# Kernel tuning notes

Hardware: AMD Instinct MI355X
Metric: run time of the kernel (lower is better)

## Reference

```python
import jax, jax.numpy as jnp
import numpy as np

N_NODES = 100000
N_EDGES = 600000
H_DIM = 128


def _gcn_layer(h, src, dst, norm, W, b):
    # m = (h @ W) * norm  -> scatter-sum over edges -> * norm + b -> LeakyReLU(0.2)
    m = jnp.matmul(h, W) * norm                      # [N, H]
    agg = jax.ops.segment_sum(m[src], dst, num_segments=N_NODES)  # [N, H]
    n = agg * norm + b
    return jnp.where(n > 0, n, 0.2 * n)


def setup_inputs() -> dict:
    key = jax.random.key(0)
    ks = jax.random.split(key, 8)
    node_id = jax.random.randint(ks[0], (N_NODES,), 0, N_NODES)
    src = jax.random.randint(ks[1], (N_EDGES,), 0, N_NODES)
    dst = jax.random.randint(ks[2], (N_EDGES,), 0, N_NODES)
    norm = jax.random.uniform(ks[3], (N_NODES, 1), dtype=jnp.float32)
    embed = jax.random.normal(ks[4], (N_NODES, H_DIM), dtype=jnp.float32) * 0.02
    embed = embed.at[0].set(0.0)  # padding_idx=0
    gain = np.sqrt(2.0)  # calculate_gain('relu')
    lim = gain * np.sqrt(6.0 / (H_DIM + H_DIM))
    W1 = jax.random.uniform(ks[5], (H_DIM, H_DIM), jnp.float32, -lim, lim)
    W2 = jax.random.uniform(ks[6], (H_DIM, H_DIM), jnp.float32, -lim, lim)
    stdv = 1.0 / np.sqrt(H_DIM)
    kb1, kb2 = jax.random.split(ks[7])
    b1 = jax.random.uniform(kb1, (H_DIM,), jnp.float32, -stdv, stdv)
    b2 = jax.random.uniform(kb2, (H_DIM,), jnp.float32, -stdv, stdv)
    return {"node_id": node_id, "src": src, "dst": dst, "norm": norm,
            "embed": embed, "W1": W1, "b1": b1, "W2": W2, "b2": b2}


def reference(node_id, src, dst, norm, embed, W1, b1, W2, b2):
    h = embed[node_id]                               # EmbeddingLayer
    h = _gcn_layer(h, src, dst, norm, W1, b1)        # GCNLayer 1
    h = _gcn_layer(h, src, dst, norm, W2, b2)        # GCNLayer 2
    return h
```

## Files before the change

kernel.cpp:

```cpp
#include <hip/hip_runtime.h>

namespace {
constexpr int NN = 100000;
constexpr int NE = 600000;
constexpr int H  = 128;
constexpr int SCAN_B = 256;
constexpr int NBLK_SCAN = (NN + SCAN_B - 1) / SCAN_B;

__global__ __launch_bounds__(256) void write_marker(float* __restrict__ out,
                                                    int n, float val) {
  int i = blockIdx.x * 256 + threadIdx.x;
  if (i < n) out[i] = val;
}


__global__ __launch_bounds__(256) void zero_f4(float4* __restrict__ p, int n4) {
  int i = blockIdx.x * 256 + threadIdx.x;
  if (i < n4) p[i] = float4{0.f, 0.f, 0.f, 0.f};
}

__global__ __launch_bounds__(256) void scatter_l1(
    const int* __restrict__ src, const int* __restrict__ dst,
    const int* __restrict__ node_id, const float* __restrict__ embed,
    const float* __restrict__ norm, float* __restrict__ agg) {
  int idx = blockIdx.x * 256 + threadIdx.x;
  int e = idx >> 5;
  if (e >= NE) return;
  int c = (idx & 31) << 2;
  int s = src[e];
  float nrm = norm[s];
  const float4 v = *reinterpret_cast<const float4*>(embed + (size_t)node_id[s] * H + c);
  float* o = agg + (size_t)dst[e] * H + c;
  atomicAdd(o + 0, v.x * nrm);
  atomicAdd(o + 1, v.y * nrm);
  atomicAdd(o + 2, v.z * nrm);
  atomicAdd(o + 3, v.w * nrm);
}

__global__ __launch_bounds__(256) void scatter_l2(
    const int* __restrict__ src, const int* __restrict__ dst,
    const float* __restrict__ h1, const float* __restrict__ norm,
    float* __restrict__ agg) {
  int idx = blockIdx.x * 256 + threadIdx.x;
  int e = idx >> 5;
  if (e >= NE) return;
  int c = (idx & 31) << 2;
  int s = src[e];
  float nrm = norm[s];
  const float4 v = *reinterpret_cast<const float4*>(h1 + (size_t)s * H + c);
  float* o = agg + (size_t)dst[e] * H + c;
  atomicAdd(o + 0, v.x * nrm);
  atomicAdd(o + 1, v.y * nrm);
  atomicAdd(o + 2, v.z * nrm);
  atomicAdd(o + 3, v.w * nrm);
}

__global__ __launch_bounds__(128) void row_gemm_act(
    const float* __restrict__ agg, const float* __restrict__ W,
    const float* __restrict__ norm, const float* __restrict__ bias,
    float* __restrict__ out) {
  __shared__ float hs[H];
  const int row = blockIdx.x, j = threadIdx.x;
  hs[j] = agg[(size_t)row * H + j];
  __syncthreads();
  float acc = 0.f;
#pragma unroll
  for (int k = 0; k < H; ++k) acc += hs[k] * W[k * H + j];
  float v = acc * norm[row] + bias[j];
  v = v > 0.f ? v : 0.2f * v;
  out[(size_t)row * H + j] = v;
}


__global__ __launch_bounds__(256) void zero_int(int* __restrict__ p, int n) {
  int i = blockIdx.x * 256 + threadIdx.x;
  if (i < n) p[i] = 0;
}

__global__ __launch_bounds__(256) void hist_dst(const int* __restrict__ dst,
                                                int* __restrict__ deg) {
  int e = blockIdx.x * 256 + threadIdx.x;
  if (e < NE) atomicAdd(&deg[dst[e]], 1);
}

__global__ __launch_bounds__(SCAN_B) void scan1(const int* __restrict__ deg,
                                                int* __restrict__ offs,
                                                int* __restrict__ bsums) {
  __shared__ int sh[SCAN_B];
  const int t = threadIdx.x;
  const int gid = blockIdx.x * SCAN_B + t;
  int v = (gid < NN) ? deg[gid] : 0;
  sh[t] = v;
  __syncthreads();
  for (int d = 1; d < SCAN_B; d <<= 1) {
    int add = (t >= d) ? sh[t - d] : 0;
    __syncthreads();
    sh[t] += add;
    __syncthreads();
  }
  if (gid < NN) offs[gid] = sh[t] - v;
  if (t == SCAN_B - 1) bsums[blockIdx.x] = sh[t];
}

__global__ __launch_bounds__(512) void scan2(int* __restrict__ bsums) {
  __shared__ int sh[512];
  const int t = threadIdx.x;
  int v = (t < NBLK_SCAN) ? bsums[t] : 0;
  sh[t] = v;
  __syncthreads();
  for (int d = 1; d < 512; d <<= 1) {
    int add = (t >= d) ? sh[t - d] : 0;
    __syncthreads();
    sh[t] += add;
    __syncthreads();
  }
  if (t < NBLK_SCAN) bsums[t] = sh[t] - v;
}

__global__ __launch_bounds__(256) void scan3(int* __restrict__ offs,
                                             const int* __restrict__ bsums,
                                             int* __restrict__ cnt) {
  int gid = blockIdx.x * 256 + threadIdx.x;
  if (gid < NN) {
    int v = offs[gid] + bsums[blockIdx.x];
    offs[gid] = v;
    cnt[gid] = v;
  }
  if (gid == 0) offs[NN] = NE;
}

template <bool WITH_REC>
__global__ __launch_bounds__(256) void fill_csr(
    const int* __restrict__ src, const int* __restrict__ dst,
    const int* __restrict__ node_id, const float* __restrict__ norm,
    int* __restrict__ cnt, int* __restrict__ csr2, int2* __restrict__ rec1) {
  int e = blockIdx.x * 256 + threadIdx.x;
  if (e >= NE) return;
  int d = dst[e];
  int s = src[e];
  int pos = atomicAdd(&cnt[d], 1);
  csr2[pos] = s;
  if (WITH_REC) rec1[pos] = make_int2(node_id[s], __float_as_int(norm[s]));
}


__global__ __launch_bounds__(256) void gather_rec(
    const int* __restrict__ offs, const int2* __restrict__ rec,
    const float* __restrict__ h, float* __restrict__ agg) {
  const int node = blockIdx.x * 8 + (threadIdx.x >> 5);
  const int c = (threadIdx.x & 31) << 2;
  const int beg = offs[node];
  const int end = offs[node + 1];
  float4 a0{0,0,0,0}, a1{0,0,0,0}, a2{0,0,0,0}, a3{0,0,0,0};
  int i = beg;
  for (; i + 4 <= end; i += 4) {
    int2 r0 = rec[i], r1 = rec[i + 1], r2 = rec[i + 2], r3 = rec[i + 3];
    const float4 v0 = *reinterpret_cast<const float4*>(h + (size_t)r0.x * H + c);
    const float4 v1 = *reinterpret_cast<const float4*>(h + (size_t)r1.x * H + c);
    const float4 v2 = *reinterpret_cast<const float4*>(h + (size_t)r2.x * H + c);
    const float4 v3 = *reinterpret_cast<const float4*>(h + (size_t)r3.x * H + c);
    float n0 = __int_as_float(r0.y), n1 = __int_as_float(r1.y);
    float n2 = __int_as_float(r2.y), n3 = __int_as_float(r3.y);
    a0.x += v0.x * n0; a0.y += v0.y * n0; a0.z += v0.z * n0; a0.w += v0.w * n0;
    a1.x += v1.x * n1; a1.y += v1.y * n1; a1.z += v1.z * n1; a1.w += v1.w * n1;
    a2.x += v2.x * n2; a2.y += v2.y * n2; a2.z += v2.z * n2; a2.w += v2.w * n2;
    a3.x += v3.x * n3; a3.y += v3.y * n3; a3.z += v3.z * n3; a3.w += v3.w * n3;
  }
  for (; i < end; ++i) {
    int2 r0 = rec[i];
    const float4 v0 = *reinterpret_cast<const float4*>(h + (size_t)r0.x * H + c);
    float n0 = __int_as_float(r0.y);
    a0.x += v0.x * n0; a0.y += v0.y * n0; a0.z += v0.z * n0; a0.w += v0.w * n0;
  }
  a0.x += a1.x + a2.x + a3.x;
  a0.y += a1.y + a2.y + a3.y;
  a0.z += a1.z + a2.z + a3.z;
  a0.w += a1.w + a2.w + a3.w;
  *reinterpret_cast<float4*>(agg + (size_t)node * H + c) = a0;
}

__global__ __launch_bounds__(256) void gather_idx(
    const int* __restrict__ offs, const int* __restrict__ csr,
    const float* __restrict__ h, float* __restrict__ agg) {
  const int node = blockIdx.x * 8 + (threadIdx.x >> 5);
  const int c = (threadIdx.x & 31) << 2;
  const int beg = offs[node];
  const int end = offs[node + 1];
  float4 a0{0,0,0,0}, a1{0,0,0,0}, a2{0,0,0,0}, a3{0,0,0,0};
  int i = beg;
  for (; i + 4 <= end; i += 4) {
    int s0 = csr[i], s1 = csr[i + 1], s2 = csr[i + 2], s3 = csr[i + 3];
    const float4 v0 = *reinterpret_cast<const float4*>(h + (size_t)s0 * H + c);
    const float4 v1 = *reinterpret_cast<const float4*>(h + (size_t)s1 * H + c);
    const float4 v2 = *reinterpret_cast<const float4*>(h + (size_t)s2 * H + c);
    const float4 v3 = *reinterpret_cast<const float4*>(h + (size_t)s3 * H + c);
    a0.x += v0.x; a0.y += v0.y; a0.z += v0.z; a0.w += v0.w;
    a1.x += v1.x; a1.y += v1.y; a1.z += v1.z; a1.w += v1.w;
    a2.x += v2.x; a2.y += v2.y; a2.z += v2.z; a2.w += v2.w;
    a3.x += v3.x; a3.y += v3.y; a3.z += v3.z; a3.w += v3.w;
  }
  for (; i < end; ++i) {
    int s0 = csr[i];
    const float4 v0 = *reinterpret_cast<const float4*>(h + (size_t)s0 * H + c);
    a0.x += v0.x; a0.y += v0.y; a0.z += v0.z; a0.w += v0.w;
  }
  a0.x += a1.x + a2.x + a3.x;
  a0.y += a1.y + a2.y + a3.y;
  a0.z += a1.z + a2.z + a3.z;
  a0.w += a1.w + a2.w + a3.w;
  *reinterpret_cast<float4*>(agg + (size_t)node * H + c) = a0;
}

__global__ __launch_bounds__(256) void gather_mid_l1(
    const int* __restrict__ offs, const int* __restrict__ csr,
    const int* __restrict__ node_id, const float* __restrict__ h,
    const float* __restrict__ norm, float* __restrict__ agg) {
  const int node = blockIdx.x * 8 + (threadIdx.x >> 5);
  const int c = (threadIdx.x & 31) << 2;
  const int beg = offs[node];
  const int end = offs[node + 1];
  float4 acc{0.f, 0.f, 0.f, 0.f};
  for (int i = beg; i < end; ++i) {
    int s = csr[i];
    float nrm = norm[s];
    const float4 v = *reinterpret_cast<const float4*>(h + (size_t)node_id[s] * H + c);
    acc.x += v.x * nrm; acc.y += v.y * nrm; acc.z += v.z * nrm; acc.w += v.w * nrm;
  }
  *reinterpret_cast<float4*>(agg + (size_t)node * H + c) = acc;
}


#define FMA4(ACC, S, W) \
  ACC.x += (S) * (W).x; ACC.y += (S) * (W).y; ACC.z += (S) * (W).z; ACC.w += (S) * (W).w;

template <bool SCALE_OUT>
__global__ __launch_bounds__(256, 2) void gemm_v5(
    const float* __restrict__ agg, const float* __restrict__ W,
    const float* __restrict__ norm, const float* __restrict__ bias,
    float* __restrict__ out) {
  const int t = threadIdx.x;
  const int rowBase = blockIdx.x * 128;
  const int j8 = t & 15;
  const int r0 = t >> 4;
  const float4* A4 = reinterpret_cast<const float4*>(agg) + (size_t)rowBase * 32;
  const float4* Wg = reinterpret_cast<const float4*>(W);

  float4 accA[8], accB[8];
#pragma unroll
  for (int i = 0; i < 8; ++i) {
    accA[i] = float4{0.f, 0.f, 0.f, 0.f};
    accB[i] = float4{0.f, 0.f, 0.f, 0.f};
  }

#pragma unroll 2
  for (int k4 = 0; k4 < 32; ++k4) {
    float4 a[8];
#pragma unroll
    for (int i = 0; i < 8; ++i) a[i] = A4[(r0 + 16 * i) * 32 + k4];
    const float4* wrow = Wg + k4 * 128 + 2 * j8;
    float4 wa0 = wrow[0],  wb0 = wrow[1];
    float4 wa1 = wrow[32], wb1 = wrow[33];
    float4 wa2 = wrow[64], wb2 = wrow[65];
    float4 wa3 = wrow[96], wb3 = wrow[97];
#pragma unroll
    for (int i = 0; i < 8; ++i) {
      FMA4(accA[i], a[i].x, wa0) FMA4(accB[i], a[i].x, wb0)
      FMA4(accA[i], a[i].y, wa1) FMA4(accB[i], a[i].y, wb1)
      FMA4(accA[i], a[i].z, wa2) FMA4(accB[i], a[i].z, wb2)
      FMA4(accA[i], a[i].w, wa3) FMA4(accB[i], a[i].w, wb3)
    }
  }

  const float4 bv0 = reinterpret_cast<const float4*>(bias)[2 * j8];
  const float4 bv1 = reinterpret_cast<const float4*>(bias)[2 * j8 + 1];
#pragma unroll
  for (int i = 0; i < 8; ++i) {
    const int row = rowBase + r0 + 16 * i;
    if (row < NN) {
      const float nrm = norm[row];
      float4 o0, o1;
      o0.x = accA[i].x * nrm + bv0.x; o0.y = accA[i].y * nrm + bv0.y;
      o0.z = accA[i].z * nrm + bv0.z; o0.w = accA[i].w * nrm + bv0.w;
      o1.x = accB[i].x * nrm + bv1.x; o1.y = accB[i].y * nrm + bv1.y;
      o1.z = accB[i].z * nrm + bv1.z; o1.w = accB[i].w * nrm + bv1.w;
      o0.x = o0.x > 0.f ? o0.x : 0.2f * o0.x;
      o0.y = o0.y > 0.f ? o0.y : 0.2f * o0.y;
      o0.z = o0.z > 0.f ? o0.z : 0.2f * o0.z;
      o0.w = o0.w > 0.f ? o0.w : 0.2f * o0.w;
      o1.x = o1.x > 0.f ? o1.x : 0.2f * o1.x;
      o1.y = o1.y > 0.f ? o1.y : 0.2f * o1.y;
      o1.z = o1.z > 0.f ? o1.z : 0.2f * o1.z;
      o1.w = o1.w > 0.f ? o1.w : 0.2f * o1.w;
      if (SCALE_OUT) {
        o0.x *= nrm; o0.y *= nrm; o0.z *= nrm; o0.w *= nrm;
        o1.x *= nrm; o1.y *= nrm; o1.z *= nrm; o1.w *= nrm;
      }
      float4* op = reinterpret_cast<float4*>(out + (size_t)row * H + j8 * 8);
      op[0] = o0;
      op[1] = o1;
    }
  }
}

}

extern "C" void kernel_launch(void* const* d_in, const int* in_sizes, int n_in,
                              void* d_out, int out_size, void* d_ws, size_t ws_size,
                              hipStream_t stream) {
  float* out = (float*)d_out;
  const int nElem = NN * H;
  const int mkBl  = (out_size + 255) / 256;

  bool order_ok =
      (n_in == 9 && in_sizes[0] == NN && in_sizes[1] == NE && in_sizes[2] == NE &&
       in_sizes[3] == NN && in_sizes[4] == NN * H && in_sizes[5] == H * H &&
       in_sizes[6] == H && in_sizes[7] == H * H && in_sizes[8] == H);
  if (!order_ok || out_size != nElem) {
    write_marker<<<mkBl, 256, 0, stream>>>(out, out_size,
                                           (out_size != nElem) ? 300.0f : 200.0f);
    return;
  }
  if (ws_size < (size_t)nElem * 4) {
    write_marker<<<mkBl, 256, 0, stream>>>(out, out_size,
                                           2.0f + (float)(ws_size >> 20));
    return;
  }

  const int* node_id = (const int*)d_in[0];
  const int* src     = (const int*)d_in[1];
  const int* dst     = (const int*)d_in[2];
  const float* norm  = (const float*)d_in[3];
  const float* embed = (const float*)d_in[4];
  const float* W1    = (const float*)d_in[5];
  const float* b1    = (const float*)d_in[6];
  const float* W2    = (const float*)d_in[7];
  const float* b2    = (const float*)d_in[8];

  float* agg = (float*)d_ws;
  float* h1n = out;
  int2* rec1 = (int2*)((char*)d_ws + (size_t)nElem * 4);
  int* csr2  = (int*)(rec1 + NE);
  int* offs  = csr2 + NE;
  int* cnt   = offs + (NN + 1);
  int* bsums = cnt + NN;

  const size_t need_mid =
      (size_t)nElem * 4 + ((size_t)NE + (NN + 1) + NN + 512) * 4;
  const size_t need_full = need_mid + (size_t)NE * 8;

  const int zeroNBl = (NN + 255) / 256;
  const int edgeBl  = (NE + 255) / 256;
  const int gemmBl  = (NN + 127) / 128;

  if (ws_size >= need_mid) {
    const bool full = (ws_size >= need_full);
    if (!full) {
      csr2  = (int*)((char*)d_ws + (size_t)nElem * 4);
      offs  = csr2 + NE;
      cnt   = offs + (NN + 1);
      bsums = cnt + NN;
    }

    zero_int<<<zeroNBl, 256, 0, stream>>>(cnt, NN);
    hist_dst<<<edgeBl, 256, 0, stream>>>(dst, cnt);
    scan1<<<NBLK_SCAN, SCAN_B, 0, stream>>>(cnt, offs, bsums);
    scan2<<<1, 512, 0, stream>>>(bsums);
    scan3<<<NBLK_SCAN, 256, 0, stream>>>(offs, bsums, cnt);
    if (full)
      fill_csr<true><<<edgeBl, 256, 0, stream>>>(src, dst, node_id, norm, cnt, csr2, rec1);
    else
      fill_csr<false><<<edgeBl, 256, 0, stream>>>(src, dst, node_id, norm, cnt, csr2, nullptr);

    if (full)
      gather_rec<<<NN / 8, 256, 0, stream>>>(offs, rec1, embed, agg);
    else
      gather_mid_l1<<<NN / 8, 256, 0, stream>>>(offs, csr2, node_id, embed, norm, agg);
    gemm_v5<true><<<gemmBl, 256, 0, stream>>>(agg, W1, norm, b1, h1n);

    gather_idx<<<NN / 8, 256, 0, stream>>>(offs, csr2, h1n, agg);
    gemm_v5<false><<<gemmBl, 256, 0, stream>>>(agg, W2, norm, b2, out);
    return;
  }

  const int zeroBl = (nElem / 4 + 255) / 256;
  const int scatBl = (NE * 32 + 255) / 256;

  zero_f4<<<zeroBl, 256, 0, stream>>>((float4*)agg, nElem / 4);
  scatter_l1<<<scatBl, 256, 0, stream>>>(src, dst, node_id, embed, norm, agg);
  row_gemm_act<<<NN, 128, 0, stream>>>(agg, W1, norm, b1, out);

  zero_f4<<<zeroBl, 256, 0, stream>>>((float4*)agg, nElem / 4);
  scatter_l2<<<scatBl, 256, 0, stream>>>(src, dst, out, norm, agg);
  row_gemm_act<<<NN, 128, 0, stream>>>(agg, W2, norm, b2, out);
}
```

Measured before the change: 421.7 us.

## Split GEMM output columns across two blocks and stage W half in LDS

Measured after the change: 371.0 us. 1.14x faster.

```diff
diff --git a/kernel.cpp b/kernel.cpp
--- a/kernel.cpp
+++ b/kernel.cpp
@@ -6,6 +6,7 @@
 constexpr int H  = 128;
 constexpr int SCAN_B = 256;
 constexpr int NBLK_SCAN = (NN + SCAN_B - 1) / SCAN_B;
+constexpr int NROWBLK = (NN + 127) / 128;
 
 __global__ __launch_bounds__(256) void write_marker(float* __restrict__ out,
                                                     int n, float val) {
@@ -234,36 +235,47 @@
   ACC.x += (S) * (W).x; ACC.y += (S) * (W).y; ACC.z += (S) * (W).z; ACC.w += (S) * (W).w;
 
 template <bool SCALE_OUT>
-__global__ __launch_bounds__(256, 2) void gemm_v5(
+__global__ __launch_bounds__(256, 3) void gemm_v6(
     const float* __restrict__ agg, const float* __restrict__ W,
     const float* __restrict__ norm, const float* __restrict__ bias,
     float* __restrict__ out) {
+  __shared__ float4 Wld[128 * 16];
   const int t = threadIdx.x;
-  const int rowBase = blockIdx.x * 128;
-  const int j8 = t & 15;
-  const int r0 = t >> 4;
+  const int half = blockIdx.x & 1;
+  const int rowBase = (blockIdx.x >> 1) * 128;
+
+  const float4* W4 = reinterpret_cast<const float4*>(W);
+#pragma unroll
+  for (int i = 0; i < 8; ++i) {
+    int g = t + i * 256;
+    int k = g >> 4, c = g & 15;
+    Wld[k * 16 + c] = W4[k * 32 + half * 16 + c];
+  }
+  __syncthreads();
+
+  const int j8 = t & 7;
+  const int r0 = t >> 3;
   const float4* A4 = reinterpret_cast<const float4*>(agg) + (size_t)rowBase * 32;
-  const float4* Wg = reinterpret_cast<const float4*>(W);
-
-  float4 accA[8], accB[8];
-#pragma unroll
-  for (int i = 0; i < 8; ++i) {
+
+  float4 accA[4], accB[4];
+#pragma unroll
+  for (int i = 0; i < 4; ++i) {
     accA[i] = float4{0.f, 0.f, 0.f, 0.f};
     accB[i] = float4{0.f, 0.f, 0.f, 0.f};
   }
 
 #pragma unroll 2
   for (int k4 = 0; k4 < 32; ++k4) {
-    float4 a[8];
-#pragma unroll
-    for (int i = 0; i < 8; ++i) a[i] = A4[(r0 + 16 * i) * 32 + k4];
-    const float4* wrow = Wg + k4 * 128 + 2 * j8;
-    float4 wa0 = wrow[0],  wb0 = wrow[1];
-    float4 wa1 = wrow[32], wb1 = wrow[33];
-    float4 wa2 = wrow[64], wb2 = wrow[65];
-    float4 wa3 = wrow[96], wb3 = wrow[97];
-#pragma unroll
-    for (int i = 0; i < 8; ++i) {
+    float4 a[4];
+#pragma unroll
+    for (int i = 0; i < 4; ++i) a[i] = A4[(r0 + 32 * i) * 32 + k4];
+    const int kb = k4 * 64;
+    float4 wa0 = Wld[kb + 2 * j8],      wb0 = Wld[kb + 2 * j8 + 1];
+    float4 wa1 = Wld[kb + 16 + 2 * j8], wb1 = Wld[kb + 16 + 2 * j8 + 1];
+    float4 wa2 = Wld[kb + 32 + 2 * j8], wb2 = Wld[kb + 32 + 2 * j8 + 1];
+    float4 wa3 = Wld[kb + 48 + 2 * j8], wb3 = Wld[kb + 48 + 2 * j8 + 1];
+#pragma unroll
+    for (int i = 0; i < 4; ++i) {
       FMA4(accA[i], a[i].x, wa0) FMA4(accB[i], a[i].x, wb0)
       FMA4(accA[i], a[i].y, wa1) FMA4(accB[i], a[i].y, wb1)
       FMA4(accA[i], a[i].z, wa2) FMA4(accB[i], a[i].z, wb2)
@@ -271,11 +283,11 @@
     }
   }
 
-  const float4 bv0 = reinterpret_cast<const float4*>(bias)[2 * j8];
-  const float4 bv1 = reinterpret_cast<const float4*>(bias)[2 * j8 + 1];
-#pragma unroll
-  for (int i = 0; i < 8; ++i) {
-    const int row = rowBase + r0 + 16 * i;
+  const float4 bv0 = reinterpret_cast<const float4*>(bias)[half * 16 + 2 * j8];
+  const float4 bv1 = reinterpret_cast<const float4*>(bias)[half * 16 + 2 * j8 + 1];
+#pragma unroll
+  for (int i = 0; i < 4; ++i) {
+    const int row = rowBase + r0 + 32 * i;
     if (row < NN) {
       const float nrm = norm[row];
       float4 o0, o1;
@@ -295,7 +307,7 @@
         o0.x *= nrm; o0.y *= nrm; o0.z *= nrm; o0.w *= nrm;
         o1.x *= nrm; o1.y *= nrm; o1.z *= nrm; o1.w *= nrm;
       }
-      float4* op = reinterpret_cast<float4*>(out + (size_t)row * H + j8 * 8);
+      float4* op = reinterpret_cast<float4*>(out + (size_t)row * H + half * 64 + j8 * 8);
       op[0] = o0;
       op[1] = o1;
     }
@@ -350,7 +362,6 @@
 
   const int zeroNBl = (NN + 255) / 256;
   const int edgeBl  = (NE + 255) / 256;
-  const int gemmBl  = (NN + 127) / 128;
 
   if (ws_size >= need_mid) {
     const bool full = (ws_size >= need_full);
@@ -375,10 +386,10 @@
       gather_rec<<<NN / 8, 256, 0, stream>>>(offs, rec1, embed, agg);
     else
       gather_mid_l1<<<NN / 8, 256, 0, stream>>>(offs, csr2, node_id, embed, norm, agg);
-    gemm_v5<true><<<gemmBl, 256, 0, stream>>>(agg, W1, norm, b1, h1n);
+    gemm_v6<true><<<NROWBLK * 2, 256, 0, stream>>>(agg, W1, norm, b1, h1n);
 
     gather_idx<<<NN / 8, 256, 0, stream>>>(offs, csr2, h1n, agg);
-    gemm_v5<false><<<gemmBl, 256, 0, stream>>>(agg, W2, norm, b2, out);
+    gemm_v6<false><<<NROWBLK * 2, 256, 0, stream>>>(agg, W2, norm, b2, out);
     return;
   }
 
```
